# Performance work log

Hardware: AMD Instinct MI355X
Metric: run time of the kernel (lower is better)

Reference implementation:

```python
import jax, jax.numpy as jnp
import numpy as np

H = 8  # heads, hard-coded in the original module


def setup_inputs() -> dict:
    key = jax.random.key(0)
    ks = jax.random.split(key, 7)
    B, Lq, Lkv = 4, 2048, 512
    dim_q, dim_kv = 1024, 768
    q = jax.random.normal(ks[0], (B, Lq, dim_q), dtype=jnp.float32)
    kv = jax.random.normal(ks[1], (B, Lkv, dim_kv), dtype=jnp.float32)
    # Linear weights stored as [in, out] so y = x @ W (math-equivalent to torch Linear)
    Wq = jax.random.normal(ks[2], (dim_q, dim_q), dtype=jnp.float32) / np.sqrt(dim_q)
    Wk = jax.random.normal(ks[3], (dim_kv, dim_q), dtype=jnp.float32) / np.sqrt(dim_kv)
    Wv = jax.random.normal(ks[4], (dim_kv, dim_q), dtype=jnp.float32) / np.sqrt(dim_kv)
    Wo = jax.random.normal(ks[5], (dim_q, dim_q), dtype=jnp.float32) / np.sqrt(dim_q)
    bo = jax.random.normal(ks[6], (dim_q,), dtype=jnp.float32) * 0.01
    return {"q": q, "kv": kv, "Wq": Wq, "Wk": Wk, "Wv": Wv, "Wo": Wo, "bo": bo}


def reference(q, kv, Wq, Wk, Wv, Wo, bo):
    B, Lq, dim_q = q.shape
    hd = dim_q // H
    scale = jnp.asarray(hd, q.dtype) ** -0.5
    # projections
    qp = q @ Wq   # [B, Lq, dim_q]
    kp = kv @ Wk  # [B, Lkv, dim_q]
    vp = kv @ Wv  # [B, Lkv, dim_q]
    # split heads: [B, L, H, hd]
    qh = qp.reshape(B, Lq, H, hd)
    kh = kp.reshape(B, kv.shape[1], H, hd)
    vh = vp.reshape(B, kv.shape[1], H, hd)
    # scaled attention scores and softmax
    scores = jnp.einsum("bqhd,bkhd->bhqk", qh, kh) * scale
    attn = jax.nn.softmax(scores, axis=-1)
    out = jnp.einsum("bhqk,bkhd->bqhd", attn, vh).reshape(B, Lq, dim_q)
    return out @ Wo + bo
```

## Files before the change

### kernel.cpp

```cpp
#include <hip/hip_runtime.h>


typedef unsigned short u16;
typedef unsigned int u32;
using short8  = __attribute__((ext_vector_type(8))) short;
using floatx4 = __attribute__((ext_vector_type(4))) float;

__device__ inline u16 f2bf(float x) {
  union { float f; u32 u; } v; v.f = x;
  u32 r = (v.u + 0x7fffu + ((v.u >> 16) & 1u)) >> 16;
  return (u16)r;
}

__device__ inline float fast_exp2(float x) {
#if __has_builtin(__builtin_amdgcn_exp2f)
  return __builtin_amdgcn_exp2f(x);
#else
  return exp2f(x);
#endif
}

#define MFMA(a, b, c) __builtin_amdgcn_mfma_f32_16x16x32_bf16(a, b, c, 0, 0, 0)

__device__ inline void async_lds16(const void* g, void* l) {
  __builtin_amdgcn_global_load_lds(
      (const __attribute__((address_space(1))) void*)g,
      (__attribute__((address_space(3))) void*)l, 16, 0, 0);
}

__global__ void cvt_all(const float* __restrict__ q, const float* __restrict__ kv,
                        u16* __restrict__ q_bf, u16* __restrict__ kv_bf) {
  int i = blockIdx.x * 256 + threadIdx.x;
  const float* src; u16* dst; int idx;
  if (i < 1048576) { src = q;  dst = q_bf;  idx = i; }
  else             { src = kv; dst = kv_bf; idx = i - 1048576; }
  float4 a = ((const float4*)src)[2 * idx];
  float4 b = ((const float4*)src)[2 * idx + 1];
  u16 t[8] = {f2bf(a.x), f2bf(a.y), f2bf(a.z), f2bf(a.w),
              f2bf(b.x), f2bf(b.y), f2bf(b.z), f2bf(b.w)};
  ((short8*)dst)[idx] = *(short8*)t;
}

__global__ __launch_bounds__(256)
void transpose_all(const float* __restrict__ Wq, const float* __restrict__ Wk,
                   const float* __restrict__ Wv, const float* __restrict__ Wo,
                   u16* __restrict__ WqT, u16* __restrict__ WkvT, u16* __restrict__ WoT) {
  __shared__ float tile[64][68];
  const int z = blockIdx.z;
  const float* W; u16* Wt; int K;
  if      (z == 0) { W = Wq; Wt = WqT;               K = 1024; }
  else if (z == 1) { W = Wk; Wt = WkvT;              K = 768;  }
  else if (z == 2) { W = Wv; Wt = WkvT + 1024 * 768; K = 768;  }
  else             { W = Wo; Wt = WoT;               K = 1024; }
  const int k0 = blockIdx.y * 64, n0 = blockIdx.x * 64;
  if (k0 >= K) return;
  const int N = 1024;
  const int t = threadIdx.x;
  for (int p = 0; p < 4; ++p) {
    int cid = p * 256 + t;
    int row = cid >> 4, c = cid & 15;
    float4 v = *(const float4*)&W[(long)(k0 + row) * N + n0 + c * 4];
    tile[row][c * 4 + 0] = v.x; tile[row][c * 4 + 1] = v.y;
    tile[row][c * 4 + 2] = v.z; tile[row][c * 4 + 3] = v.w;
  }
  __syncthreads();
  for (int p = 0; p < 2; ++p) {
    int oc = p * 256 + t;
    int n = oc >> 3, c = oc & 7;
    u16 tmp[8];
    for (int s = 0; s < 8; ++s) tmp[s] = f2bf(tile[c * 8 + s][n]);
    *(short8*)&Wt[(long)(n0 + n) * K + k0 + c * 8] = *(short8*)tmp;
  }
}

__global__ __launch_bounds__(256)
void gemm_bt(const u16* __restrict__ A, const u16* __restrict__ Bt,
             u16* __restrict__ Cb, float* __restrict__ Cf,
             const float* __restrict__ bias, u16* __restrict__ vt_out,
             int M, int N, int K, int ldc, int mt_per_xcd) {
  __shared__ u16 smem[17664];
  u16* As = smem;
  u16* Bs = smem + 8192;
  const int tid  = threadIdx.x;
  const int wave = tid >> 6, lane = tid & 63;
  const int l15  = lane & 15, quad = lane >> 4;
  const int wm   = (wave >> 1) * 64, wn = (wave & 1) * 64;
  const int lin  = blockIdx.x;
  const int xcd  = lin & 7, slot = lin >> 3;
  const int mt   = xcd * mt_per_xcd + (slot % mt_per_xcd);
  const int nti  = slot / mt_per_xcd;
  const long m0  = (long)mt * 128, n0 = (long)nti * 128;
  const int lrow = lane >> 3;
  const int lk   = (lane & 7) * 8;

  floatx4 acc[4][4] = {};

  for (int k0 = 0; k0 < K; k0 += 64) {
    for (int c = 0; c < 4; ++c) {
      int rbase = (wave * 4 + c) * 8;
      async_lds16(A  + (m0 + rbase + lrow) * (long)K + k0 + lk, &As[(wave * 4 + c) * 512]);
      async_lds16(Bt + (n0 + rbase + lrow) * (long)K + k0 + lk, &Bs[(wave * 4 + c) * 512]);
    }
    __syncthreads();
    for (int kc = 0; kc < 2; ++kc) {
      short8 af[4], bfr[4];
      for (int i = 0; i < 4; ++i)
        af[i] = *(const short8*)&As[(wm + i * 16 + l15) * 64 + kc * 32 + quad * 8];
      for (int j = 0; j < 4; ++j)
        bfr[j] = *(const short8*)&Bs[(wn + j * 16 + l15) * 64 + kc * 32 + quad * 8];
      for (int i = 0; i < 4; ++i)
        for (int j = 0; j < 4; ++j)
          acc[i][j] = MFMA(af[i], bfr[j], acc[i][j]);
    }
    __syncthreads();
  }

  if (Cf) {
    for (int i = 0; i < 4; ++i)
      for (int j = 0; j < 4; ++j) {
        long row = m0 + wm + i * 16 + quad * 4;
        long col = n0 + wn + j * 16 + l15;
        float b = bias ? bias[col] : 0.f;
        for (int r = 0; r < 4; ++r) Cf[(row + r) * (long)ldc + col] = acc[i][j][r] + b;
      }
    return;
  }
  for (int i = 0; i < 4; ++i)
    for (int j = 0; j < 4; ++j)
      for (int r = 0; r < 4; ++r)
        smem[(wm + i * 16 + quad * 4 + r) * 138 + wn + j * 16 + l15] = f2bf(acc[i][j][r]);
  __syncthreads();
  if (vt_out && nti >= 8) {
    const int h  = nti - 8;
    const int bq = (int)(m0 >> 9);
    const int l0 = (int)(m0 & 511);
    u16* vbase = vt_out + ((long)(bq * 8 + h) * 128) * 512;
    for (int p = 0; p < 8; ++p) {
      int cid = p * 256 + tid;
      int d = cid >> 4, c = cid & 15;
      u16 tmp[8];
      for (int s = 0; s < 8; ++s) tmp[s] = smem[(c * 8 + s) * 138 + d];
      *(short8*)&vbase[(long)d * 512 + l0 + c * 8] = *(short8*)tmp;
    }
  } else {
    for (int p = 0; p < 8; ++p) {
      int cid = p * 256 + tid;
      int row = cid >> 4, c = cid & 15;
      short8 v = *(const short8*)&smem[row * 138 + c * 8];
      *(short8*)&Cb[(m0 + row) * (long)ldc + n0 + c * 8] = v;
    }
  }
}

__global__ __launch_bounds__(256, 4)
void attn_kernel(const u16* __restrict__ qp, const u16* __restrict__ kp,
                 const u16* __restrict__ vT, u16* __restrict__ ctx) {
  __shared__ u16 Ks[64 * 128];
  __shared__ u16 Vs[128 * 64];
  __shared__ u16 Pb[4][16 * 64];
  const int tid  = threadIdx.x;
  const int wave = tid >> 6, lane = tid & 63;
  const int l15  = lane & 15, quad = lane >> 4;
  const int lin  = blockIdx.x;
  const int xcd  = lin & 7, slot = lin >> 3;
  const int pairIdx = xcd * 4 + (slot & 3);
  const int b = pairIdx >> 3, h = pairIdx & 7;
  const int qtile = slot >> 2;
  const long rowbase = (long)b * 2048 + qtile * 64 + wave * 16;
  const float sc = 0.08838834764831845f * 1.4426950408889634f;

  short8 aQ[4];
  for (int dc = 0; dc < 4; ++dc)
    aQ[dc] = *(const short8*)&qp[(rowbase + l15) * 1024 + h * 128 + dc * 32 + quad * 8];

  floatx4 O[8] = {};
  float lsum[4] = {};
  const u16* kpb   = kp + ((long)b * 512) * 1024 + h * 128;
  const u16* vbase = vT + ((long)(b * 8 + h) * 128) * 512;

  const int krow = lane >> 4;
  const int kpos = lane & 15;
  const int vrow = lane >> 3;
  const int vpos = lane & 7;

  for (int t = 0; t < 8; ++t) {
    for (int i = 0; i < 4; ++i) {
      int inst = wave * 4 + i;
      int row  = inst * 4 + krow;
      int g    = kpos ^ (row & 15);
      async_lds16(kpb + (long)(t * 64 + row) * 1024 + g * 8, &Ks[inst * 512]);
    }
    for (int i = 0; i < 4; ++i) {
      int inst = wave * 4 + i;
      int d    = inst * 8 + vrow;
      int g    = vpos ^ (d & 7);
      async_lds16(vbase + (long)d * 512 + t * 64 + g * 8, &Vs[inst * 512]);
    }
    __syncthreads();

    floatx4 S[4] = {};
    for (int dc = 0; dc < 4; ++dc)
      for (int ks = 0; ks < 4; ++ks) {
        int k = ks * 16 + l15;
        short8 bk = *(const short8*)&Ks[k * 128 + (((dc * 4 + quad) ^ l15) * 8)];
        S[ks] = MFMA(aQ[dc], bk, S[ks]);
      }
    for (int ks = 0; ks < 4; ++ks)
      for (int r = 0; r < 4; ++r) {
        float p = fast_exp2(S[ks][r] * sc);
        lsum[r] += p;
        int row = quad * 4 + r;
        int g   = (ks * 2 + (l15 >> 3)) ^ (row & 7);
        Pb[wave][row * 64 + g * 8 + (l15 & 7)] = f2bf(p);
      }
    short8 aP[2];
    for (int kc = 0; kc < 2; ++kc)
      aP[kc] = *(const short8*)&Pb[wave][l15 * 64 + (((kc * 4 + quad) ^ (l15 & 7)) * 8)];
    for (int j = 0; j < 8; ++j) {
      int d = j * 16 + l15;
      short8 bV0 = *(const short8*)&Vs[d * 64 + ((quad ^ (l15 & 7)) * 8)];
      short8 bV1 = *(const short8*)&Vs[d * 64 + (((4 + quad) ^ (l15 & 7)) * 8)];
      O[j] = MFMA(aP[0], bV0, O[j]);
      O[j] = MFMA(aP[1], bV1, O[j]);
    }
    __syncthreads();
  }

  for (int r = 0; r < 4; ++r) {
    float sum = lsum[r];
    for (int off = 1; off < 16; off <<= 1) sum += __shfl_xor(sum, off);
    lsum[r] = 1.f / sum;
  }
  for (int j = 0; j < 8; ++j)
    for (int r = 0; r < 4; ++r)
      ctx[(rowbase + quad * 4 + r) * 1024 + h * 128 + j * 16 + l15] =
          f2bf(O[j][r] * lsum[r]);
}

extern "C" void kernel_launch(void* const* d_in, const int* in_sizes, int n_in,
                              void* d_out, int out_size, void* d_ws, size_t ws_size,
                              hipStream_t stream) {
  const float* q  = (const float*)d_in[0];
  const float* kv = (const float*)d_in[1];
  const float* Wq = (const float*)d_in[2];
  const float* Wk = (const float*)d_in[3];
  const float* Wv = (const float*)d_in[4];
  const float* Wo = (const float*)d_in[5];
  const float* bo = (const float*)d_in[6];
  float* out = (float*)d_out;

  char* ws = (char*)d_ws;
  u16* q_bf  = (u16*)(ws + 0);
  u16* kv_bf = (u16*)(ws + 16777216);
  u16* WqT   = (u16*)(ws + 19922944);
  u16* WkvT  = (u16*)(ws + 22020096);
  u16* WoT   = (u16*)(ws + 25165824);
  u16* qp    = (u16*)(ws + 27262976);
  u16* kp    = (u16*)(ws + 44040192);
  u16* vT    = (u16*)(ws + 52428800);
  u16* ctx   = (u16*)(ws + 56623104);

  cvt_all<<<4864, 256, 0, stream>>>(q, kv, q_bf, kv_bf);
  transpose_all<<<dim3(16, 16, 4), 256, 0, stream>>>(Wq, Wk, Wv, Wo, WqT, WkvT, WoT);

  gemm_bt<<<512, 256, 0, stream>>>(q_bf, WqT, qp, nullptr, nullptr, nullptr,
                                   8192, 1024, 1024, 1024, 8);
  gemm_bt<<<256, 256, 0, stream>>>(kv_bf, WkvT, kp, nullptr, nullptr, vT,
                                   2048, 2048, 768, 1024, 2);

  attn_kernel<<<1024, 256, 0, stream>>>(qp, kp, vT, ctx);

  gemm_bt<<<512, 256, 0, stream>>>(ctx, WoT, nullptr, out, bo, nullptr,
                                   8192, 1024, 1024, 1024, 8);
}
```

Measured before the change: 211.9 us.

## Fuse projection, attention and output GEMMs into one cooperative persistent kernel

Combines the Q and KV projection GEMMs, the attention kernel and the output projection into a single cooperative kernel of 1024 blocks, separated by grid-wide syncs. The Q and KV projections now run concurrently in the first phase instead of as separate launches. This removes kernel launch gaps and lets the two projections overlap. In exchange, the GEMM phases run under the attention kernel's launch bounds and LDS size, so some blocks sit idle during those phases. A fallback path with separate kernels is used when the occupancy query reports fewer than 4 blocks per CU.

```diff
diff --git a/kernel.cpp b/kernel.cpp
--- a/kernel.cpp
+++ b/kernel.cpp
@@ -1,4 +1,7 @@
 #include <hip/hip_runtime.h>
+#include <hip/hip_cooperative_groups.h>
+
+namespace cg = cooperative_groups;
 
 
 typedef unsigned short u16;
@@ -73,19 +76,17 @@
   }
 }
 
-__global__ __launch_bounds__(256)
-void gemm_bt(const u16* __restrict__ A, const u16* __restrict__ Bt,
-             u16* __restrict__ Cb, float* __restrict__ Cf,
-             const float* __restrict__ bias, u16* __restrict__ vt_out,
-             int M, int N, int K, int ldc, int mt_per_xcd) {
-  __shared__ u16 smem[17664];
+__device__ __forceinline__
+void gemm_body(const u16* __restrict__ A, const u16* __restrict__ Bt,
+               u16* __restrict__ Cb, float* __restrict__ Cf,
+               const float* __restrict__ bias, u16* __restrict__ vt_out,
+               int K, int ldc, int lin, int mt_per_xcd, u16* smem) {
   u16* As = smem;
   u16* Bs = smem + 8192;
   const int tid  = threadIdx.x;
   const int wave = tid >> 6, lane = tid & 63;
   const int l15  = lane & 15, quad = lane >> 4;
   const int wm   = (wave >> 1) * 64, wn = (wave & 1) * 64;
-  const int lin  = blockIdx.x;
   const int xcd  = lin & 7, slot = lin >> 3;
   const int mt   = xcd * mt_per_xcd + (slot % mt_per_xcd);
   const int nti  = slot / mt_per_xcd;
@@ -152,16 +153,16 @@
   }
 }
 
-__global__ __launch_bounds__(256, 4)
-void attn_kernel(const u16* __restrict__ qp, const u16* __restrict__ kp,
-                 const u16* __restrict__ vT, u16* __restrict__ ctx) {
-  __shared__ u16 Ks[64 * 128];
-  __shared__ u16 Vs[128 * 64];
-  __shared__ u16 Pb[4][16 * 64];
+__device__ __forceinline__
+void attn_body(const u16* __restrict__ qp, const u16* __restrict__ kp,
+               const u16* __restrict__ vT, u16* __restrict__ ctx,
+               int lin, u16* smem) {
+  u16* Ks = smem;
+  u16* Vs = smem + 8192;
   const int tid  = threadIdx.x;
   const int wave = tid >> 6, lane = tid & 63;
+  u16* Pw = smem + 16384 + wave * 1024;
   const int l15  = lane & 15, quad = lane >> 4;
-  const int lin  = blockIdx.x;
   const int xcd  = lin & 7, slot = lin >> 3;
   const int pairIdx = xcd * 4 + (slot & 3);
   const int b = pairIdx >> 3, h = pairIdx & 7;
@@ -211,11 +212,11 @@
         lsum[r] += p;
         int row = quad * 4 + r;
         int g   = (ks * 2 + (l15 >> 3)) ^ (row & 7);
-        Pb[wave][row * 64 + g * 8 + (l15 & 7)] = f2bf(p);
+        Pw[row * 64 + g * 8 + (l15 & 7)] = f2bf(p);
       }
     short8 aP[2];
     for (int kc = 0; kc < 2; ++kc)
-      aP[kc] = *(const short8*)&Pb[wave][l15 * 64 + (((kc * 4 + quad) ^ (l15 & 7)) * 8)];
+      aP[kc] = *(const short8*)&Pw[l15 * 64 + (((kc * 4 + quad) ^ (l15 & 7)) * 8)];
     for (int j = 0; j < 8; ++j) {
       int d = j * 16 + l15;
       short8 bV0 = *(const short8*)&Vs[d * 64 + ((quad ^ (l15 & 7)) * 8)];
@@ -235,6 +236,52 @@
     for (int r = 0; r < 4; ++r)
       ctx[(rowbase + quad * 4 + r) * 1024 + h * 128 + j * 16 + l15] =
           f2bf(O[j][r] * lsum[r]);
+}
+
+__global__ __launch_bounds__(256, 4)
+void mega(const u16* q_bf, const u16* WqT, const u16* kv_bf, const u16* WkvT,
+          const u16* WoT, u16* qp, u16* kp, u16* vT, u16* ctx,
+          float* out, const float* bo) {
+  __shared__ u16 smem[20480];
+  cg::grid_group g = cg::this_grid();
+  const int bid = blockIdx.x;
+
+  if (bid < 768) {
+    const bool isQ = bid < 512;
+    gemm_body(isQ ? q_bf : kv_bf, isQ ? WqT : WkvT, isQ ? qp : kp,
+              nullptr, nullptr, isQ ? (u16*)nullptr : vT,
+              isQ ? 1024 : 768, 1024, isQ ? bid : bid - 512, isQ ? 8 : 2, smem);
+  }
+  g.sync();
+  attn_body(qp, kp, vT, ctx, bid, smem);
+  g.sync();
+  if (bid < 512)
+    gemm_body(ctx, WoT, nullptr, out, bo, nullptr, 1024, 1024, bid, 8, smem);
+}
+
+__global__ __launch_bounds__(256)
+void k_proj_q(const u16* __restrict__ q_bf, const u16* __restrict__ WqT,
+              u16* __restrict__ qp) {
+  __shared__ u16 smem[17664];
+  gemm_body(q_bf, WqT, qp, nullptr, nullptr, nullptr, 1024, 1024, blockIdx.x, 8, smem);
+}
+__global__ __launch_bounds__(256)
+void k_proj_kv(const u16* __restrict__ kv_bf, const u16* __restrict__ WkvT,
+               u16* __restrict__ kp, u16* __restrict__ vT) {
+  __shared__ u16 smem[17664];
+  gemm_body(kv_bf, WkvT, kp, nullptr, nullptr, vT, 768, 1024, blockIdx.x, 2, smem);
+}
+__global__ __launch_bounds__(256, 4)
+void k_attn(const u16* __restrict__ qp, const u16* __restrict__ kp,
+            const u16* __restrict__ vT, u16* __restrict__ ctx) {
+  __shared__ u16 smem[20480];
+  attn_body(qp, kp, vT, ctx, blockIdx.x, smem);
+}
+__global__ __launch_bounds__(256)
+void k_oproj(const u16* __restrict__ ctx, const u16* __restrict__ WoT,
+             float* __restrict__ out, const float* __restrict__ bo) {
+  __shared__ u16 smem[17664];
+  gemm_body(ctx, WoT, nullptr, out, bo, nullptr, 1024, 1024, blockIdx.x, 8, smem);
 }
 
 extern "C" void kernel_launch(void* const* d_in, const int* in_sizes, int n_in,
@@ -263,13 +310,19 @@
   cvt_all<<<4864, 256, 0, stream>>>(q, kv, q_bf, kv_bf);
   transpose_all<<<dim3(16, 16, 4), 256, 0, stream>>>(Wq, Wk, Wv, Wo, WqT, WkvT, WoT);
 
-  gemm_bt<<<512, 256, 0, stream>>>(q_bf, WqT, qp, nullptr, nullptr, nullptr,
-                                   8192, 1024, 1024, 1024, 8);
-  gemm_bt<<<256, 256, 0, stream>>>(kv_bf, WkvT, kp, nullptr, nullptr, vT,
-                                   2048, 2048, 768, 1024, 2);
-
-  attn_kernel<<<1024, 256, 0, stream>>>(qp, kp, vT, ctx);
-
-  gemm_bt<<<512, 256, 0, stream>>>(ctx, WoT, nullptr, out, bo, nullptr,
-                                   8192, 1024, 1024, 1024, 8);
-}
+  int maxb = 0;
+  hipError_t oe = hipOccupancyMaxActiveBlocksPerMultiprocessor(
+      &maxb, (const void*)mega, 256, 0);
+  if (oe == hipSuccess && maxb >= 4) {
+    void* args[] = {(void*)&q_bf, (void*)&WqT, (void*)&kv_bf, (void*)&WkvT,
+                    (void*)&WoT, (void*)&qp, (void*)&kp, (void*)&vT,
+                    (void*)&ctx, (void*)&out, (void*)&bo};
+    hipLaunchCooperativeKernel((const void*)mega, dim3(1024), dim3(256),
+                               args, 0, stream);
+  } else {
+    k_proj_q<<<512, 256, 0, stream>>>(q_bf, WqT, qp);
+    k_proj_kv<<<256, 256, 0, stream>>>(kv_bf, WkvT, kp, vT);
+    k_attn<<<1024, 256, 0, stream>>>(qp, kp, vT, ctx);
+    k_oproj<<<512, 256, 0, stream>>>(ctx, WoT, out, bo);
+  }
+}
```

New measurement: 211.2 us. About the same (-0.4%).
